# Kernel tuning notes

Measured on AMD Instinct MI355X. Metric: run time of the kernel, lower is better.

## Reference

```python
import jax, jax.numpy as jnp
import numpy as np

K = 1024
R = 4            # grid_rows * grid_cols = 2*2
D_IN = 128
D_HID = 256
D_OUT = 64
HEADS = 4
ALPHA = 0.2      # LeakyReLU slope
SEM_TH = 0.7


def _normalize(x, axis=-1):
    # torch F.normalize: x / max(||x||, eps)
    n = jnp.linalg.norm(x, axis=axis, keepdims=True)
    return x / jnp.maximum(n, 1e-12)


def _build_adjacency(page_vectors, page_numbers):
    KR = K * R
    N = K + KR + 1
    pv = _normalize(page_vectors.astype(jnp.float32))
    ps = pv @ pv.T                                    # (K,K) cosine sims
    eye_k = jnp.eye(K, dtype=bool)
    A_pp = jnp.where((ps >= SEM_TH) & (~eye_k), ps, 0.0)
    pn = page_numbers
    adj_pn = jnp.abs(pn[:, None] - pn[None, :]) == 1  # consecutive pages
    A_pp = jnp.where(adj_pn, jnp.maximum(A_pp, 0.8), A_pp)
    g_page = jnp.arange(KR) // R                      # owning page of each region
    A_pr = (g_page[None, :] == jnp.arange(K)[:, None]).astype(jnp.float32)  # (K,KR)
    same_pg = (g_page[:, None] == g_page[None, :]) & (~jnp.eye(KR, dtype=bool))
    A_rr = jnp.where(same_pg, 0.9, 0.0)
    adj = jnp.zeros((N, N), dtype=jnp.float32)
    adj = adj.at[:K, :K].set(A_pp)
    adj = adj.at[:K, K:K + KR].set(A_pr)
    adj = adj.at[K:K + KR, :K].set(A_pr.T)
    adj = adj.at[K:K + KR, K:K + KR].set(A_rr)
    adj = adj.at[N - 1, :N - 1].set(1.0)              # query node fully connected
    adj = adj.at[:N - 1, N - 1].set(1.0)
    adj = adj + jnp.eye(N, dtype=jnp.float32)         # self loops
    adj = adj / jnp.maximum(adj.sum(axis=1, keepdims=True), 1e-8)
    return adj


def _gat_layer(h, adj, W, a_src, a_dst, concat):
    # Standard multi-head GAT: e_ij = LeakyReLU(a_src.Wh_i + a_dst.Wh_j)
    N = h.shape[0]
    H, F_out = a_src.shape
    Wh = (h @ W).reshape(N, H, F_out)
    s = jnp.einsum('nhf,hf->nh', Wh, a_src)           # (N,H)
    d = jnp.einsum('nhf,hf->nh', Wh, a_dst)
    e = jax.nn.leaky_relu(s[:, None, :] + d[None, :, :], ALPHA)  # (N,N,H)
    e = jnp.where((adj > 0)[:, :, None], e, -1e9)
    att = jax.nn.softmax(e, axis=1)
    out = jnp.einsum('ijh,jhf->ihf', att, Wh)
    if concat:
        return jax.nn.elu(out.reshape(N, H * F_out))
    return out.mean(axis=1)


def setup_inputs() -> dict:
    key = jax.random.key(0)
    ks = jax.random.split(key, 20)
    sc = 0.05
    inp = {
        'page_vectors': jax.random.normal(ks[0], (K, D_IN), jnp.float32),
        'region_vectors': jax.random.normal(ks[1], (K * R, D_IN), jnp.float32),
        'query_vector': jax.random.normal(ks[2], (D_IN,), jnp.float32),
        'page_numbers': jnp.arange(K, dtype=jnp.int64) if jax.config.jax_enable_x64 else jnp.arange(K, dtype=jnp.int32),
        'stage1_scores': jax.random.normal(ks[3], (K,), jnp.float32),
        # input_proj
        'W_in': jax.random.normal(ks[4], (D_IN, D_HID), jnp.float32) * sc,
        'b_in': jnp.zeros((D_HID,), jnp.float32),
        # GAT layer 0: in=hidden, out=hidden, concat
        'W_g0': jax.random.normal(ks[5], (D_HID, HEADS * D_HID), jnp.float32) * sc,
        'a_src0': jax.random.normal(ks[6], (HEADS, D_HID), jnp.float32) * sc,
        'a_dst0': jax.random.normal(ks[7], (HEADS, D_HID), jnp.float32) * sc,
        # GAT layer 1: in=hidden*heads, out=output_dim, average
        'W_g1': jax.random.normal(ks[8], (D_HID * HEADS, HEADS * D_OUT), jnp.float32) * sc,
        'a_src1': jax.random.normal(ks[9], (HEADS, D_OUT), jnp.float32) * sc,
        'a_dst1': jax.random.normal(ks[10], (HEADS, D_OUT), jnp.float32) * sc,
        # residual proj
        'W_res': jax.random.normal(ks[11], (D_HID, D_OUT), jnp.float32) * sc,
        'b_res': jnp.zeros((D_OUT,), jnp.float32),
        # score head
        'W_s1': jax.random.normal(ks[12], (2 * D_OUT, D_OUT), jnp.float32) * sc,
        'b_s1': jnp.zeros((D_OUT,), jnp.float32),
        'W_s2': jax.random.normal(ks[13], (D_OUT, 1), jnp.float32) * sc,
        'b_s2': jnp.zeros((1,), jnp.float32),
        'lambda_mix': jnp.asarray(0.5, jnp.float32),
    }
    return inp


def reference(page_vectors, region_vectors, query_vector, page_numbers, stage1_scores,
              W_in, b_in, W_g0, a_src0, a_dst0, W_g1, a_src1, a_dst1,
              W_res, b_res, W_s1, b_s1, W_s2, b_s2, lambda_mix):
    q = _normalize(query_vector.astype(jnp.float32)[None, :])
    node_feats = _normalize(jnp.concatenate([page_vectors, region_vectors, q], axis=0))
    adj = _build_adjacency(page_vectors, page_numbers)
    h = node_feats @ W_in + b_in
    h_res = h
    h = _gat_layer(h, adj, W_g0, a_src0, a_dst0, concat=True)
    h = _gat_layer(h, adj, W_g1, a_src1, a_dst1, concat=False)
    h = h + (h_res @ W_res + b_res)
    page_repr = h[:K]                              # (K, D_OUT)
    query_repr = h[K + K * R]                      # (D_OUT,)
    pair = jnp.concatenate([page_repr, jnp.broadcast_to(query_repr, (K, D_OUT))], axis=-1)
    delta = (jax.nn.relu(pair @ W_s1 + b_s1) @ W_s2 + b_s2)[:, 0]
    s0 = stage1_scores.astype(jnp.float32)
    s0 = (s0 - s0.min()) / (s0.max() - s0.min() + 1e-8)
    lam = jax.nn.sigmoid(lambda_mix)
    return (1.0 - lam) * s0 + lam * delta
```

## Files before the change

kernel.cpp:

```cpp
#include <hip/hip_runtime.h>
#include <math.h>

#define KPG    1024
#define KRN    4096
#define NN     5121
#define MPAD   5184
#define DIN    128
#define DHID   256
#define DOUT   64
#define NHEAD  4
#define LALPHA 0.2f
#define SEMTH  0.7f
#define QNB0   128
#define QCH0   ((NN + QNB0 - 1) / QNB0)
#define QNB1   128
#define QCH1   ((NN + QNB1 - 1) / QNB1)
#define MAXD   32
#define NBLK_NORM ((NN + 1) / 2)

typedef __bf16 bf16x8 __attribute__((ext_vector_type(8)));
typedef float  f32x4  __attribute__((ext_vector_type(4)));

__device__ __forceinline__ float wave_sum(float v){
  #pragma unroll
  for (int o = 32; o > 0; o >>= 1) v += __shfl_down(v, o, 64);
  return v;
}

__device__ __forceinline__ float lrelu(float x){ return x >= 0.f ? x : LALPHA * x; }

__device__ __forceinline__ void tobf(float v, __bf16& h, __bf16& l){
  h = (__bf16)v;
  l = (__bf16)(v - (float)h);
}

__device__ __forceinline__ void xcd_bxy(int& bx, int& by){
  int nwg = gridDim.x * gridDim.y;
  int orig = blockIdx.y * gridDim.x + blockIdx.x;
  int q = nwg >> 3, r = nwg & 7, xcd = orig & 7, idx = orig >> 3;
  int wg = (xcd < r ? xcd * (q + 1) : r * (q + 1) + (xcd - r) * q) + idx;
  bx = wg % gridDim.x;
  by = wg / gridDim.x;
}

__global__ __launch_bounds__(256) void k_prep(const float* __restrict__ pv,
                                              const float* __restrict__ rv,
                                              const float* __restrict__ qv,
                                              const float* __restrict__ Win,
                                              const float* __restrict__ Wg0,
                                              const float* __restrict__ Wg1,
                                              __bf16* __restrict__ nfH,
                                              __bf16* __restrict__ nfL,
                                              __bf16* __restrict__ WinH,
                                              __bf16* __restrict__ Wg0H,
                                              __bf16* __restrict__ Wg1H){
  __shared__ float tile[64][65];
  __shared__ float w4[4];
  int b = blockIdx.x, t = threadIdx.x;
  if (b < NBLK_NORM){
    int i = b * 2 + (t >> 7);
    int tt = t & 127;
    float x = 0.f;
    if (i < NN){
      const float* src = (i < KPG) ? pv + (size_t)i * DIN
                       : (i < KPG + KRN) ? rv + (size_t)(i - KPG) * DIN : qv;
      x = src[tt];
    }
    float ss = wave_sum(x * x);
    if ((t & 63) == 0) w4[t >> 6] = ss;
    __syncthreads();
    if (i < NN){
      int rh = t >> 7;
      float norm = sqrtf(w4[2 * rh] + w4[2 * rh + 1]);
      float y = x / fmaxf(norm, 1e-12f);
      __bf16 h, l; tobf(y, h, l);
      nfH[(size_t)i * DIN + tt] = h;
      nfL[(size_t)i * DIN + tt] = l;
    }
  } else {
    int bb = b - NBLK_NORM;
    const float* W; __bf16 *TH; int K, N, tb;
    if (bb < 8){ W = Win; TH = WinH; K = DIN;  N = DHID; tb = bb; }
    else if (bb < 72){ W = Wg0; TH = Wg0H; K = DHID; N = 1024; tb = bb - 8; }
    else { W = Wg1; TH = Wg1H; K = 1024; N = DHID; tb = bb - 72; }
    int ntx = N >> 6;
    int kb = (tb / ntx) * 64, nb = (tb % ntx) * 64;
    int rr = t >> 6, cc = t & 63;
    #pragma unroll
    for (int i = 0; i < 16; ++i){
      int k = i * 4 + rr;
      tile[k][cc] = W[(size_t)(kb + k) * N + nb + cc];
    }
    __syncthreads();
    #pragma unroll
    for (int i = 0; i < 16; ++i){
      int n = i * 4 + rr;
      TH[(size_t)(nb + n) * K + kb + cc] = (__bf16)tile[cc][n];
    }
  }
}

#define MFMA(a,b,c) __builtin_amdgcn_mfma_f32_16x16x32_bf16(a, b, c, 0, 0, 0)

struct Acc { f32x4 a00, a01, a10, a11; };

template<int K, bool X3>
__device__ __forceinline__ Acc gemm_core(const __bf16* __restrict__ AH,
                                         const __bf16* __restrict__ AL,
                                         const __bf16* __restrict__ BH,
                                         const __bf16* __restrict__ BL,
                                         int rblk, int cblk,
                                         __bf16* sm){
  int t = threadIdx.x, w = t >> 6, l = t & 63;
  int lr = l & 15, lk = l >> 4;
  __bf16* sAh = sm;
  __bf16* sBh = sm + 4096;
  __bf16* sAl = sm + 8192;
  __bf16* sBl = sm + 12288;

  int srow = t >> 3, scol = t & 7;
  int e0 = srow * 64 + ((scol ^ (srow & 7)) * 8);
  int e1 = e0 + 32 * 64;
  size_t gA0 = (size_t)(rblk + srow) * K + scol * 8;
  size_t gA1 = gA0 + (size_t)32 * K;
  size_t gB0 = (size_t)(cblk + srow) * K + scol * 8;
  size_t gB1 = gB0 + (size_t)32 * K;

  int ar0 = (w >> 1) * 32 + lr, ar1 = ar0 + 16;
  int bc0 = (w & 1) * 32 + lr,  bc1 = bc0 + 16;

  Acc acc;
  #pragma unroll
  for (int r = 0; r < 4; ++r){ acc.a00[r]=0.f; acc.a01[r]=0.f; acc.a10[r]=0.f; acc.a11[r]=0.f; }

  int4 st0, st1, st4, st5, st2, st3, st6, st7;
  st0 = *(const int4*)(AH + gA0);
  st1 = *(const int4*)(AH + gA1);
  st4 = *(const int4*)(BH + gB0);
  st5 = *(const int4*)(BH + gB1);
  if (X3){
    st2 = *(const int4*)(AL + gA0);
    st3 = *(const int4*)(AL + gA1);
    st6 = *(const int4*)(BL + gB0);
    st7 = *(const int4*)(BL + gB1);
  }

  const int NSTEP = K / 64;
  #pragma unroll 1
  for (int s = 0; s < NSTEP; ++s){
    __syncthreads();
    *(int4*)(sAh + e0) = st0;  *(int4*)(sAh + e1) = st1;
    *(int4*)(sBh + e0) = st4;  *(int4*)(sBh + e1) = st5;
    if (X3){
      *(int4*)(sAl + e0) = st2;  *(int4*)(sAl + e1) = st3;
      *(int4*)(sBl + e0) = st6;  *(int4*)(sBl + e1) = st7;
    }
    if (s + 1 < NSTEP){
      size_t ka = (size_t)(s + 1) * 64;
      st0 = *(const int4*)(AH + gA0 + ka);
      st1 = *(const int4*)(AH + gA1 + ka);
      st4 = *(const int4*)(BH + gB0 + ka);
      st5 = *(const int4*)(BH + gB1 + ka);
      if (X3){
        st2 = *(const int4*)(AL + gA0 + ka);
        st3 = *(const int4*)(AL + gA1 + ka);
        st6 = *(const int4*)(BL + gB0 + ka);
        st7 = *(const int4*)(BL + gB1 + ka);
      }
    }
    __syncthreads();
    #pragma unroll
    for (int kk = 0; kk < 2; ++kk){
      int pc = ((lk + kk * 4) ^ (lr & 7)) * 8;
      bf16x8 A0h = *(const bf16x8*)(sAh + ar0 * 64 + pc);
      bf16x8 A1h = *(const bf16x8*)(sAh + ar1 * 64 + pc);
      bf16x8 B0h = *(const bf16x8*)(sBh + bc0 * 64 + pc);
      bf16x8 B1h = *(const bf16x8*)(sBh + bc1 * 64 + pc);
      acc.a00 = MFMA(A0h, B0h, acc.a00);
      acc.a01 = MFMA(A0h, B1h, acc.a01);
      acc.a10 = MFMA(A1h, B0h, acc.a10);
      acc.a11 = MFMA(A1h, B1h, acc.a11);
      if (X3){
        bf16x8 A0l = *(const bf16x8*)(sAl + ar0 * 64 + pc);
        bf16x8 A1l = *(const bf16x8*)(sAl + ar1 * 64 + pc);
        bf16x8 B0l = *(const bf16x8*)(sBl + bc0 * 64 + pc);
        bf16x8 B1l = *(const bf16x8*)(sBl + bc1 * 64 + pc);
        acc.a00 = MFMA(A0h, B0l, acc.a00); acc.a00 = MFMA(A0l, B0h, acc.a00);
        acc.a01 = MFMA(A0h, B1l, acc.a01); acc.a01 = MFMA(A0l, B1h, acc.a01);
        acc.a10 = MFMA(A1h, B0l, acc.a10); acc.a10 = MFMA(A1l, B0h, acc.a10);
        acc.a11 = MFMA(A1h, B1l, acc.a11); acc.a11 = MFMA(A1l, B1h, acc.a11);
      }
    }
  }
  return acc;
}

template<int K, bool BIAS, bool WF32, bool WBF16>
__global__ __launch_bounds__(256) void k_gemm3(const __bf16* __restrict__ AH,
                                               const __bf16* __restrict__ BH,
                                               const float* __restrict__ bias,
                                               float* __restrict__ Cf,
                                               __bf16* __restrict__ Cb,
                                               int N){
  __shared__ __bf16 smem[8192];
  int bx, by; xcd_bxy(bx, by);
  int rblk = by * 64, cblk = bx * 64;
  Acc acc = gemm_core<K, false>(AH, nullptr, BH, nullptr, rblk, cblk, smem);
  int t = threadIdx.x, w = t >> 6, l = t & 63;
  int lr = l & 15, lk = l >> 4;
  int rb = rblk + (w >> 1) * 32 + lk * 4;
  int cb = cblk + (w & 1) * 32 + lr;
  #pragma unroll
  for (int m = 0; m < 2; ++m){
    #pragma unroll
    for (int n = 0; n < 2; ++n){
      const f32x4& a = (m == 0) ? (n == 0 ? acc.a00 : acc.a01) : (n == 0 ? acc.a10 : acc.a11);
      int col = cb + n * 16;
      float bv = BIAS ? bias[col] : 0.f;
      #pragma unroll
      for (int r = 0; r < 4; ++r){
        int row = rb + m * 16 + r;
        float v = a[r] + bv;
        size_t o = (size_t)row * N + col;
        if (WF32) Cf[o] = v;
        if (WBF16) Cb[o] = (__bf16)v;
      }
    }
  }
}

template<int K, bool BIAS, bool WF32, bool WBF16>
__global__ __launch_bounds__(512) void k_gemm3s(const __bf16* __restrict__ AH,
                                                const __bf16* __restrict__ BH,
                                                const float* __restrict__ bias,
                                                float* __restrict__ Cf,
                                                __bf16* __restrict__ Cb,
                                                int N){
  __shared__ __bf16 smem[16384];
  int bx, by; xcd_bxy(bx, by);
  int rblk = by * 64, cblk = bx * 64;
  int t = threadIdx.x, kq = t >> 8, tl = t & 255;
  int w = t >> 6, quad = w & 3, l = t & 63;
  int lr = l & 15, lk = l >> 4;
  const int KH = K / 2;
  int kbase = kq * KH;

  __bf16* sAh = smem + kq * 8192;
  __bf16* sBh = sAh + 4096;

  int srow = tl >> 3, scol = tl & 7;
  int e0 = srow * 64 + ((scol ^ (srow & 7)) * 8);
  int e1 = e0 + 32 * 64;
  size_t gA0 = (size_t)(rblk + srow) * K + kbase + scol * 8;
  size_t gA1 = gA0 + (size_t)32 * K;
  size_t gB0 = (size_t)(cblk + srow) * K + kbase + scol * 8;
  size_t gB1 = gB0 + (size_t)32 * K;

  int ar0 = (quad >> 1) * 32 + lr, ar1 = ar0 + 16;
  int bc0 = (quad & 1) * 32 + lr,  bc1 = bc0 + 16;

  Acc acc;
  #pragma unroll
  for (int r = 0; r < 4; ++r){ acc.a00[r]=0.f; acc.a01[r]=0.f; acc.a10[r]=0.f; acc.a11[r]=0.f; }

  int4 st0 = *(const int4*)(AH + gA0);
  int4 st1 = *(const int4*)(AH + gA1);
  int4 st4 = *(const int4*)(BH + gB0);
  int4 st5 = *(const int4*)(BH + gB1);

  const int NSTEP = KH / 64;
  #pragma unroll 1
  for (int s = 0; s < NSTEP; ++s){
    __syncthreads();
    *(int4*)(sAh + e0) = st0;  *(int4*)(sAh + e1) = st1;
    *(int4*)(sBh + e0) = st4;  *(int4*)(sBh + e1) = st5;
    if (s + 1 < NSTEP){
      size_t ka = (size_t)(s + 1) * 64;
      st0 = *(const int4*)(AH + gA0 + ka);
      st1 = *(const int4*)(AH + gA1 + ka);
      st4 = *(const int4*)(BH + gB0 + ka);
      st5 = *(const int4*)(BH + gB1 + ka);
    }
    __syncthreads();
    #pragma unroll
    for (int kk = 0; kk < 2; ++kk){
      int pc = ((lk + kk * 4) ^ (lr & 7)) * 8;
      bf16x8 A0h = *(const bf16x8*)(sAh + ar0 * 64 + pc);
      bf16x8 A1h = *(const bf16x8*)(sAh + ar1 * 64 + pc);
      bf16x8 B0h = *(const bf16x8*)(sBh + bc0 * 64 + pc);
      bf16x8 B1h = *(const bf16x8*)(sBh + bc1 * 64 + pc);
      acc.a00 = MFMA(A0h, B0h, acc.a00);
      acc.a01 = MFMA(A0h, B1h, acc.a01);
      acc.a10 = MFMA(A1h, B0h, acc.a10);
      acc.a11 = MFMA(A1h, B1h, acc.a11);
    }
  }

  __syncthreads();
  float* part = (float*)smem;
  int rbase = (quad >> 1) * 32, cbase = (quad & 1) * 32;
  #pragma unroll
  for (int m = 0; m < 2; ++m){
    #pragma unroll
    for (int n = 0; n < 2; ++n){
      const f32x4& a = (m == 0) ? (n == 0 ? acc.a00 : acc.a01) : (n == 0 ? acc.a10 : acc.a11);
      #pragma unroll
      for (int r = 0; r < 4; ++r)
        part[kq * 4096 + (rbase + m * 16 + lk * 4 + r) * 64 + cbase + n * 16 + lr] = a[r];
    }
  }
  __syncthreads();
  #pragma unroll
  for (int e = 0; e < 8; ++e){
    int idx = e * 512 + t;
    int row = idx >> 6, col = idx & 63;
    float v = part[idx] + part[4096 + idx];
    if (BIAS) v += bias[cblk + col];
    size_t o = (size_t)(rblk + row) * N + cblk + col;
    if (WF32) Cf[o] = v;
    if (WBF16) Cb[o] = (__bf16)v;
  }
}

__global__ __launch_bounds__(256) void k_sim3(const __bf16* __restrict__ nfH,
                                              const __bf16* __restrict__ nfL,
                                              const int* __restrict__ pn,
                                              unsigned char* __restrict__ mask){
  __shared__ __bf16 smem[16384];
  int bx, by; xcd_bxy(bx, by);
  int rblk = by * 64, cblk = bx * 64;
  Acc acc = gemm_core<DIN, true>(nfH, nfL, nfH, nfL, rblk, cblk, smem);
  int t = threadIdx.x, w = t >> 6, l = t & 63;
  int lr = l & 15, lk = l >> 4;
  int rb = rblk + (w >> 1) * 32 + lk * 4;
  int cb = cblk + (w & 1) * 32 + lr;
  #pragma unroll
  for (int m = 0; m < 2; ++m){
    #pragma unroll
    for (int n = 0; n < 2; ++n){
      const f32x4& a = (m == 0) ? (n == 0 ? acc.a00 : acc.a01) : (n == 0 ? acc.a10 : acc.a11);
      int j = cb + n * 16;
      int pnj = pn[j];
      #pragma unroll
      for (int r = 0; r < 4; ++r){
        int i = rb + m * 16 + r;
        float s = a[r];
        int d = pn[i] - pnj;
        bool mb = ((s >= SEMTH) && (j != i)) || (d == 1) || (d == -1) || (j == i);
        mask[(size_t)i * KPG + j] = mb ? 1 : 0;
      }
    }
  }
}

__global__ __launch_bounds__(64) void k_nbr(const unsigned char* __restrict__ mask,
                                            int* __restrict__ nbr,
                                            int* __restrict__ deg){
  int i = blockIdx.x, l = threadIdx.x;
  const unsigned char* mrow = mask + (size_t)i * KPG;
  int off = 0;
  #pragma unroll
  for (int c = 0; c < 16; ++c){
    int j = c * 64 + l;
    bool b = mrow[j] != 0;
    unsigned long long bal = __ballot(b);
    int pos = off + __popcll(bal & ((1ull << l) - 1ull));
    if (b && pos < MAXD) nbr[i * MAXD + pos] = j;
    off += __popcll(bal);
  }
  if (l == 0) deg[i] = (off > MAXD) ? MAXD : off;
}

__global__ __launch_bounds__(256) void k_sd0(const __bf16* __restrict__ wh,
                                             const float* __restrict__ asrc,
                                             const float* __restrict__ adst,
                                             float* __restrict__ sd){
  int n = blockIdx.x, t = threadIdx.x, hh = t >> 6, l = t & 63;
  float s = 0.f, d = 0.f;
  #pragma unroll
  for (int k = 0; k < 4; ++k){
    int idx = hh * 256 + k * 64 + l;
    float v = (float)wh[(size_t)n * 1024 + idx];
    s += v * asrc[idx];
    d += v * adst[idx];
  }
  s = wave_sum(s); d = wave_sum(d);
  if (l == 0){ sd[n * 8 + hh] = s; sd[n * 8 + 4 + hh] = d; }
}

__global__ __launch_bounds__(256) void k_gat0all(const __bf16* __restrict__ wh,
                                                 const float* __restrict__ sd,
                                                 const int* __restrict__ nbr,
                                                 const int* __restrict__ deg,
                                                 __bf16* __restrict__ h1H,
                                                 float* __restrict__ qpart,
                                                 float* __restrict__ qz){
  int b = blockIdx.x, t = threadIdx.x;
  if (b < QNB0){
    int bq = b;
    float sq[NHEAD];
    #pragma unroll
    for (int h = 0; h < NHEAD; ++h) sq[h] = sd[(size_t)(NN - 1) * 8 + h];
    int j0 = bq * QCH0, j1 = (j0 + QCH0 < NN) ? j0 + QCH0 : NN;
    float acc[NHEAD] = {0.f, 0.f, 0.f, 0.f};
    float z[NHEAD] = {0.f, 0.f, 0.f, 0.f};
    #pragma unroll 4
    for (int j = j0; j < j1; ++j){
      float4 d4 = *(const float4*)&sd[j * 8 + 4];
      float e0 = expf(lrelu(sq[0] + d4.x));
      float e1 = expf(lrelu(sq[1] + d4.y));
      float e2 = expf(lrelu(sq[2] + d4.z));
      float e3 = expf(lrelu(sq[3] + d4.w));
      z[0] += e0; z[1] += e1; z[2] += e2; z[3] += e3;
      size_t base = (size_t)j * 1024 + t;
      acc[0] += e0 * (float)wh[base];
      acc[1] += e1 * (float)wh[base + 256];
      acc[2] += e2 * (float)wh[base + 512];
      acc[3] += e3 * (float)wh[base + 768];
    }
    #pragma unroll
    for (int h = 0; h < NHEAD; ++h) qpart[(size_t)bq * 1024 + h * 256 + t] = acc[h];
    if (t == 0){
      #pragma unroll
      for (int h = 0; h < NHEAD; ++h) qz[bq * 4 + h] = z[h];
    }
  } else if (b < QNB0 + KPG){
    int i = b - QNB0;
    __shared__ int jl[MAXD + 5];
    __shared__ float wgt[NHEAD][MAXD + 5];
    __shared__ float izs[NHEAD];
    int nd = deg[i], cnt = nd + 5;
    if (t < cnt)
      jl[t] = (t < nd) ? nbr[i * MAXD + t]
                       : ((t < nd + 4) ? (KPG + 4 * i + (t - nd)) : (NN - 1));
    __syncthreads();
    if (t < 4 * cnt){
      int x = t >> 2, h = t & 3;
      wgt[h][x] = expf(lrelu(sd[i * 8 + h] + sd[jl[x] * 8 + 4 + h]));
    }
    __syncthreads();
    if (t < NHEAD){
      float Z = 0.f;
      for (int x = 0; x < cnt; ++x) Z += wgt[t][x];
      izs[t] = 1.f / Z;
    }
    __syncthreads();
    float acc[NHEAD] = {0.f, 0.f, 0.f, 0.f};
    #pragma unroll 4
    for (int x = 0; x < cnt; ++x){
      size_t base = (size_t)jl[x] * 1024 + t;
      #pragma unroll
      for (int h = 0; h < NHEAD; ++h) acc[h] += wgt[h][x] * (float)wh[base + h * 256];
    }
    size_t ob = (size_t)i * 1024;
    #pragma unroll
    for (int h = 0; h < NHEAD; ++h){
      float v = acc[h] * izs[h];
      v = (v > 0.f) ? v : expm1f(v);
      h1H[ob + h * 256 + t] = (__bf16)v;
    }
  } else {
    int g = b - QNB0 - KPG;
    __shared__ float wgt2[4][NHEAD][6];
    int rb = KPG + 4 * g;
    if (t < 16){
      int r = t >> 2, h = t & 3;
      int i = rb + r;
      float si = sd[i * 8 + h];
      int jx[6] = {g, rb, rb + 1, rb + 2, rb + 3, NN - 1};
      float Z = 0.f, e[6];
      #pragma unroll
      for (int x = 0; x < 6; ++x){
        e[x] = expf(lrelu(si + sd[jx[x] * 8 + 4 + h]));
        Z += e[x];
      }
      float iz = 1.f / Z;
      #pragma unroll
      for (int x = 0; x < 6; ++x) wgt2[r][h][x] = e[x] * iz;
    }
    __syncthreads();
    float acc[4][NHEAD] = {};
    int jx[6] = {g, rb, rb + 1, rb + 2, rb + 3, NN - 1};
    #pragma unroll
    for (int x = 0; x < 6; ++x){
      size_t base = (size_t)jx[x] * 1024 + t;
      #pragma unroll
      for (int h = 0; h < NHEAD; ++h){
        float v = (float)wh[base + h * 256];
        #pragma unroll
        for (int r = 0; r < 4; ++r) acc[r][h] += wgt2[r][h][x] * v;
      }
    }
    #pragma unroll
    for (int r = 0; r < 4; ++r){
      size_t ob = (size_t)(rb + r) * 1024;
      #pragma unroll
      for (int h = 0; h < NHEAD; ++h){
        float v = acc[r][h];
        v = (v > 0.f) ? v : expm1f(v);
        h1H[ob + h * 256 + t] = (__bf16)v;
      }
    }
  }
}

__global__ __launch_bounds__(256) void k_qfin0(const float* __restrict__ qpart,
                                               const float* __restrict__ qz,
                                               __bf16* __restrict__ h1H){
  int h = blockIdx.x, t = threadIdx.x;
  float s = 0.f, Z = 0.f;
  #pragma unroll 4
  for (int b = 0; b < QNB0; ++b){
    s += qpart[(size_t)b * 1024 + h * 256 + t];
    Z += qz[b * 4 + h];
  }
  float v = s / Z;
  v = (v > 0.f) ? v : expm1f(v);
  h1H[(size_t)(NN - 1) * 1024 + h * 256 + t] = (__bf16)v;
}

__global__ __launch_bounds__(256) void k_sd1(const __bf16* __restrict__ wh,
                                             const float* __restrict__ asrc,
                                             const float* __restrict__ adst,
                                             float* __restrict__ sd){
  int n = blockIdx.x, t = threadIdx.x, hh = t >> 6, l = t & 63;
  float v = (float)wh[(size_t)n * 256 + hh * 64 + l];
  float s = wave_sum(v * asrc[hh * 64 + l]);
  float d = wave_sum(v * adst[hh * 64 + l]);
  if (l == 0){ sd[n * 8 + hh] = s; sd[n * 8 + 4 + hh] = d; }
}

__global__ __launch_bounds__(256) void k_gat1all(const __bf16* __restrict__ wh,
                                                 const float* __restrict__ sd,
                                                 const int* __restrict__ nbr,
                                                 const int* __restrict__ deg,
                                                 float* __restrict__ h2,
                                                 float* __restrict__ qpart,
                                                 float* __restrict__ qz){
  int b = blockIdx.x, t = threadIdx.x, hh = t >> 6;
  if (b < QNB1){
    int bq = b;
    float sq = sd[(size_t)(NN - 1) * 8 + hh];
    int j0 = bq * QCH1, j1 = (j0 + QCH1 < NN) ? j0 + QCH1 : NN;
    float acc = 0.f, z = 0.f;
    #pragma unroll 4
    for (int j = j0; j < j1; ++j){
      float e = expf(lrelu(sq + sd[j * 8 + 4 + hh]));
      z += e;
      acc += e * (float)wh[(size_t)j * 256 + t];
    }
    qpart[(size_t)bq * 256 + t] = acc;
    if ((t & 63) == 0) qz[bq * 4 + hh] = z;
  } else {
    int i = b - QNB1;
    __shared__ int jl[MAXD + 5];
    __shared__ float wgt[NHEAD][MAXD + 5];
    __shared__ float izs[NHEAD];
    int nd = deg[i], cnt = nd + 5;
    if (t < cnt)
      jl[t] = (t < nd) ? nbr[i * MAXD + t]
                       : ((t < nd + 4) ? (KPG + 4 * i + (t - nd)) : (NN - 1));
    __syncthreads();
    if (t < 4 * cnt){
      int x = t >> 2, h = t & 3;
      wgt[h][x] = expf(lrelu(sd[i * 8 + h] + sd[jl[x] * 8 + 4 + h]));
    }
    __syncthreads();
    if (t < NHEAD){
      float Z = 0.f;
      for (int x = 0; x < cnt; ++x) Z += wgt[t][x];
      izs[t] = 1.f / Z;
    }
    __syncthreads();
    float acc = 0.f;
    #pragma unroll 4
    for (int x = 0; x < cnt; ++x)
      acc += wgt[hh][x] * (float)wh[(size_t)jl[x] * 256 + t];
    acc *= izs[hh];
    __shared__ float col[256];
    col[t] = acc;
    __syncthreads();
    if (t < 64)
      h2[(size_t)i * 64 + t] = 0.25f * (col[t] + col[64 + t] + col[128 + t] + col[192 + t]);
  }
}

__global__ __launch_bounds__(256) void k_qfin1mm(const float* __restrict__ qpart,
                                                 const float* __restrict__ qz,
                                                 const float* __restrict__ s0,
                                                 float* __restrict__ h2,
                                                 float* __restrict__ mm){
  int t = threadIdx.x, hh = t >> 6;
  float mn = 1e30f, mx = -1e30f;
  for (int j = t; j < KPG; j += 256){
    float v = s0[j];
    mn = fminf(mn, v); mx = fmaxf(mx, v);
  }
  __shared__ float smn[256], smx[256];
  smn[t] = mn; smx[t] = mx;
  __syncthreads();
  for (int s = 128; s > 0; s >>= 1){
    if (t < s){ smn[t] = fminf(smn[t], smn[t + s]); smx[t] = fmaxf(smx[t], smx[t + s]); }
    __syncthreads();
  }
  if (t == 0){ mm[0] = smn[0]; mm[1] = smx[0]; }
  float s = 0.f, Z = 0.f;
  #pragma unroll 4
  for (int b = 0; b < QNB1; ++b){
    s += qpart[(size_t)b * 256 + t];
    Z += qz[b * 4 + hh];
  }
  __shared__ float col[256];
  col[t] = s / Z;
  __syncthreads();
  if (t < 64)
    h2[(size_t)KPG * 64 + t] = 0.25f * (col[t] + col[64 + t] + col[128 + t] + col[192 + t]);
}

__global__ __launch_bounds__(64) void k_score2(const float* __restrict__ h2,
                                               const float* __restrict__ hres,
                                               const float* __restrict__ Wres,
                                               const float* __restrict__ bres,
                                               const float* __restrict__ Ws1,
                                               const float* __restrict__ bs1,
                                               const float* __restrict__ Ws2,
                                               const float* __restrict__ bs2,
                                               const float* __restrict__ s0,
                                               const float* __restrict__ lmix,
                                               const float* __restrict__ mm,
                                               float* __restrict__ out){
  int i = blockIdx.x, t = threadIdx.x;
  __shared__ float hrow[DHID], hq[DHID], pg[64], qr[64];
  #pragma unroll
  for (int k = 0; k < 4; ++k){
    hrow[k * 64 + t] = hres[(size_t)i * DHID + k * 64 + t];
    hq[k * 64 + t]   = hres[(size_t)(NN - 1) * DHID + k * 64 + t];
  }
  __syncthreads();
  float ri = bres[t], rq = bres[t];
  #pragma unroll 8
  for (int d = 0; d < DHID; ++d){
    float w = Wres[d * 64 + t];
    ri += hrow[d] * w;
    rq += hq[d] * w;
  }
  pg[t] = h2[(size_t)i * 64 + t] + ri;
  qr[t] = h2[(size_t)KPG * 64 + t] + rq;
  __syncthreads();
  float z = bs1[t];
  #pragma unroll 8
  for (int d = 0; d < 64; ++d){
    z += pg[d] * Ws1[d * 64 + t];
    z += qr[d] * Ws1[(64 + d) * 64 + t];
  }
  z = fmaxf(z, 0.f);
  float v = wave_sum(z * Ws2[t]);
  if (t == 0){
    float delta = v + bs2[0];
    float mn = mm[0], mx = mm[1];
    float s0n = (s0[i] - mn) / (mx - mn + 1e-8f);
    float lam = 1.f / (1.f + expf(-lmix[0]));
    out[i] = (1.f - lam) * s0n + lam * delta;
  }
}

extern "C" void kernel_launch(void* const* d_in, const int* in_sizes, int n_in,
                              void* d_out, int out_size, void* d_ws, size_t ws_size,
                              hipStream_t stream){
  const float* pv  = (const float*)d_in[0];
  const float* rv  = (const float*)d_in[1];
  const float* qv  = (const float*)d_in[2];
  const int*   pn  = (const int*)d_in[3];
  const float* s0  = (const float*)d_in[4];
  const float* Win = (const float*)d_in[5];
  const float* bin = (const float*)d_in[6];
  const float* Wg0 = (const float*)d_in[7];
  const float* as0 = (const float*)d_in[8];
  const float* ad0 = (const float*)d_in[9];
  const float* Wg1 = (const float*)d_in[10];
  const float* as1 = (const float*)d_in[11];
  const float* ad1 = (const float*)d_in[12];
  const float* Wrs = (const float*)d_in[13];
  const float* brs = (const float*)d_in[14];
  const float* Ws1 = (const float*)d_in[15];
  const float* bs1 = (const float*)d_in[16];
  const float* Ws2 = (const float*)d_in[17];
  const float* bs2 = (const float*)d_in[18];
  const float* lmx = (const float*)d_in[19];
  float* out = (float*)d_out;

  float* ws = (float*)d_ws;
  size_t off = 0;
  __bf16* nfH = (__bf16*)(ws + off); off += (size_t)MPAD * DIN / 2;
  __bf16* nfL = (__bf16*)(ws + off); off += (size_t)MPAD * DIN / 2;
  __bf16* WinH = (__bf16*)(ws + off); off += (size_t)DHID * DIN / 2;
  __bf16* Wg0H = (__bf16*)(ws + off); off += (size_t)1024 * DHID / 2;
  __bf16* Wg1H = (__bf16*)(ws + off); off += (size_t)DHID * 1024 / 2;
  float* hres = ws + off; off += (size_t)MPAD * DHID;
  __bf16* hresH = (__bf16*)(ws + off); off += (size_t)MPAD * DHID / 2;
  __bf16* wh0H = (__bf16*)(ws + off); off += (size_t)MPAD * 1024 / 2;
  __bf16* h1H  = (__bf16*)(ws + off); off += (size_t)MPAD * 1024 / 2;
  __bf16* wh1H = (__bf16*)(ws + off); off += (size_t)MPAD * 256 / 2;
  float* sd0  = ws + off; off += (size_t)NN * 8;
  float* sd1  = ws + off; off += (size_t)NN * 8;
  float* h2   = ws + off; off += (size_t)(KPG + 1) * 64;
  float* qp0  = ws + off; off += (size_t)QNB0 * 1024;
  float* qp1  = ws + off; off += (size_t)QNB1 * 256;
  float* qz0  = ws + off; off += (size_t)QNB0 * 4;
  float* qz1  = ws + off; off += (size_t)QNB1 * 4;
  float* mm   = ws + off; off += 8;
  int*   nbr  = (int*)(ws + off); off += (size_t)KPG * MAXD;
  int*   deg  = (int*)(ws + off); off += KPG;
  unsigned char* mask = (unsigned char*)(ws + off);

  k_prep<<<NBLK_NORM + 136, 256, 0, stream>>>(pv, rv, qv, Win, Wg0, Wg1,
                                              nfH, nfL, WinH, Wg0H, Wg1H);
  k_sim3<<<dim3(16, 16), 256, 0, stream>>>(nfH, nfL, pn, mask);
  k_nbr<<<KPG, 64, 0, stream>>>(mask, nbr, deg);
  k_gemm3s<DIN, true, true, true><<<dim3(4, 81), 512, 0, stream>>>(
      nfH, WinH, bin, hres, hresH, DHID);
  k_gemm3<DHID, false, false, true><<<dim3(16, 81), 256, 0, stream>>>(
      hresH, Wg0H, nullptr, nullptr, wh0H, 1024);
  k_sd0<<<NN, 256, 0, stream>>>(wh0H, as0, ad0, sd0);
  k_gat0all<<<QNB0 + 2 * KPG, 256, 0, stream>>>(wh0H, sd0, nbr, deg, h1H, qp0, qz0);
  k_qfin0<<<NHEAD, 256, 0, stream>>>(qp0, qz0, h1H);
  k_gemm3s<1024, false, false, true><<<dim3(4, 81), 512, 0, stream>>>(
      h1H, Wg1H, nullptr, nullptr, wh1H, DHID);
  k_sd1<<<NN, 256, 0, stream>>>(wh1H, as1, ad1, sd1);
  k_gat1all<<<QNB1 + KPG, 256, 0, stream>>>(wh1H, sd1, nbr, deg, h2, qp1, qz1);
  k_qfin1mm<<<1, 256, 0, stream>>>(qp1, qz1, s0, h2, mm);
  k_score2<<<KPG, 64, 0, stream>>>(h2, hres, Wrs, brs, Ws1, bs1, Ws2, bs2, s0, lmx, mm, out);
}
```

Before: 114.1 us.

## Merge independent kernels and fold query finalization into last-block epilogues

Launches are fused horizontally: the similarity-mask GEMM runs alongside the input projection GEMM, and neighbor-list extraction runs alongside the Wg0 GEMM, each dispatched by block index. The separate query-finalization kernels are removed, and the last block to finish (tracked by an atomic counter zeroed in k_prep) performs that reduction instead. This cuts the launch count from 13 to 9 and the serialized gaps between launches. expf is also replaced with __expf. The risk is that the threadfence and atomic ordering must hold, and the fast exp is slightly less accurate.

```diff
diff --git a/kernel.cpp b/kernel.cpp
--- a/kernel.cpp
+++ b/kernel.cpp
@@ -34,13 +34,9 @@
   l = (__bf16)(v - (float)h);
 }
 
-__device__ __forceinline__ void xcd_bxy(int& bx, int& by){
-  int nwg = gridDim.x * gridDim.y;
-  int orig = blockIdx.y * gridDim.x + blockIdx.x;
+__device__ __forceinline__ int swz_lin(int orig, int nwg){
   int q = nwg >> 3, r = nwg & 7, xcd = orig & 7, idx = orig >> 3;
-  int wg = (xcd < r ? xcd * (q + 1) : r * (q + 1) + (xcd - r) * q) + idx;
-  bx = wg % gridDim.x;
-  by = wg / gridDim.x;
+  return (xcd < r ? xcd * (q + 1) : r * (q + 1) + (xcd - r) * q) + idx;
 }
 
 __global__ __launch_bounds__(256) void k_prep(const float* __restrict__ pv,
@@ -53,10 +49,12 @@
                                               __bf16* __restrict__ nfL,
                                               __bf16* __restrict__ WinH,
                                               __bf16* __restrict__ Wg0H,
-                                              __bf16* __restrict__ Wg1H){
+                                              __bf16* __restrict__ Wg1H,
+                                              unsigned int* __restrict__ gcnt){
   __shared__ float tile[64][65];
   __shared__ float w4[4];
   int b = blockIdx.x, t = threadIdx.x;
+  if (b == 0 && t < 8) gcnt[t] = 0;
   if (b < NBLK_NORM){
     int i = b * 2 + (t >> 7);
     int tt = t & 127;
@@ -195,49 +193,120 @@
   return acc;
 }
 
-template<int K, bool BIAS, bool WF32, bool WBF16>
-__global__ __launch_bounds__(256) void k_gemm3(const __bf16* __restrict__ AH,
-                                               const __bf16* __restrict__ BH,
-                                               const float* __restrict__ bias,
-                                               float* __restrict__ Cf,
-                                               __bf16* __restrict__ Cb,
-                                               int N){
+__global__ __launch_bounds__(256) void k_simhres(const __bf16* __restrict__ nfH,
+                                                 const __bf16* __restrict__ nfL,
+                                                 const int* __restrict__ pn,
+                                                 const __bf16* __restrict__ WinH,
+                                                 const float* __restrict__ bin,
+                                                 unsigned char* __restrict__ mask,
+                                                 float* __restrict__ hres,
+                                                 __bf16* __restrict__ hresH){
+  __shared__ __bf16 smem[16384];
+  int b = blockIdx.x, t = threadIdx.x;
+  int w = t >> 6, l = t & 63, lr = l & 15, lk = l >> 4;
+  if (b < 256){
+    int wg = swz_lin(b, 256);
+    int rblk = (wg >> 4) * 64, cblk = (wg & 15) * 64;
+    Acc acc = gemm_core<DIN, true>(nfH, nfL, nfH, nfL, rblk, cblk, smem);
+    int rb = rblk + (w >> 1) * 32 + lk * 4;
+    int cb = cblk + (w & 1) * 32 + lr;
+    #pragma unroll
+    for (int m = 0; m < 2; ++m){
+      #pragma unroll
+      for (int n = 0; n < 2; ++n){
+        const f32x4& a = (m == 0) ? (n == 0 ? acc.a00 : acc.a01) : (n == 0 ? acc.a10 : acc.a11);
+        int j = cb + n * 16;
+        int pnj = pn[j];
+        #pragma unroll
+        for (int r = 0; r < 4; ++r){
+          int i = rb + m * 16 + r;
+          float s = a[r];
+          int d = pn[i] - pnj;
+          bool mb = ((s >= SEMTH) && (j != i)) || (d == 1) || (d == -1) || (j == i);
+          mask[(size_t)i * KPG + j] = mb ? 1 : 0;
+        }
+      }
+    }
+  } else {
+    int bb = swz_lin(b - 256, 324);
+    int rblk = (bb >> 2) * 64, cblk = (bb & 3) * 64;
+    Acc acc = gemm_core<DIN, false>(nfH, nullptr, WinH, nullptr, rblk, cblk, smem);
+    int rb = rblk + (w >> 1) * 32 + lk * 4;
+    int cb = cblk + (w & 1) * 32 + lr;
+    #pragma unroll
+    for (int m = 0; m < 2; ++m){
+      #pragma unroll
+      for (int n = 0; n < 2; ++n){
+        const f32x4& a = (m == 0) ? (n == 0 ? acc.a00 : acc.a01) : (n == 0 ? acc.a10 : acc.a11);
+        int col = cb + n * 16;
+        float bv = bin[col];
+        #pragma unroll
+        for (int r = 0; r < 4; ++r){
+          int row = rb + m * 16 + r;
+          float v = a[r] + bv;
+          size_t o = (size_t)row * DHID + col;
+          hres[o] = v;
+          hresH[o] = (__bf16)v;
+        }
+      }
+    }
+  }
+}
+
+__global__ __launch_bounds__(256) void k_nbrwh0(const __bf16* __restrict__ hresH,
+                                                const __bf16* __restrict__ Wg0H,
+                                                const unsigned char* __restrict__ mask,
+                                                __bf16* __restrict__ wh0H,
+                                                int* __restrict__ nbr,
+                                                int* __restrict__ deg){
   __shared__ __bf16 smem[8192];
-  int bx, by; xcd_bxy(bx, by);
-  int rblk = by * 64, cblk = bx * 64;
-  Acc acc = gemm_core<K, false>(AH, nullptr, BH, nullptr, rblk, cblk, smem);
-  int t = threadIdx.x, w = t >> 6, l = t & 63;
-  int lr = l & 15, lk = l >> 4;
-  int rb = rblk + (w >> 1) * 32 + lk * 4;
-  int cb = cblk + (w & 1) * 32 + lr;
-  #pragma unroll
-  for (int m = 0; m < 2; ++m){
-    #pragma unroll
-    for (int n = 0; n < 2; ++n){
-      const f32x4& a = (m == 0) ? (n == 0 ? acc.a00 : acc.a01) : (n == 0 ? acc.a10 : acc.a11);
-      int col = cb + n * 16;
-      float bv = BIAS ? bias[col] : 0.f;
-      #pragma unroll
-      for (int r = 0; r < 4; ++r){
-        int row = rb + m * 16 + r;
-        float v = a[r] + bv;
-        size_t o = (size_t)row * N + col;
-        if (WF32) Cf[o] = v;
-        if (WBF16) Cb[o] = (__bf16)v;
-      }
-    }
-  }
-}
-
-template<int K, bool BIAS, bool WF32, bool WBF16>
+  int b = blockIdx.x, t = threadIdx.x;
+  if (b < 1296){
+    int wg = swz_lin(b, 1296);
+    int rblk = (wg >> 4) * 64, cblk = (wg & 15) * 64;
+    Acc acc = gemm_core<DHID, false>(hresH, nullptr, Wg0H, nullptr, rblk, cblk, smem);
+    int w = t >> 6, l = t & 63, lr = l & 15, lk = l >> 4;
+    int rb = rblk + (w >> 1) * 32 + lk * 4;
+    int cb = cblk + (w & 1) * 32 + lr;
+    #pragma unroll
+    for (int m = 0; m < 2; ++m){
+      #pragma unroll
+      for (int n = 0; n < 2; ++n){
+        const f32x4& a = (m == 0) ? (n == 0 ? acc.a00 : acc.a01) : (n == 0 ? acc.a10 : acc.a11);
+        int col = cb + n * 16;
+        #pragma unroll
+        for (int r = 0; r < 4; ++r)
+          wh0H[(size_t)(rb + m * 16 + r) * 1024 + col] = (__bf16)a[r];
+      }
+    }
+  } else {
+    int i = (b - 1296) * 4 + (t >> 6);
+    int l = t & 63;
+    const unsigned char* mrow = mask + (size_t)i * KPG;
+    int off = 0;
+    #pragma unroll
+    for (int c = 0; c < 16; ++c){
+      int j = c * 64 + l;
+      bool bb = mrow[j] != 0;
+      unsigned long long bal = __ballot(bb);
+      int pos = off + __popcll(bal & ((1ull << l) - 1ull));
+      if (bb && pos < MAXD) nbr[i * MAXD + pos] = j;
+      off += __popcll(bal);
+    }
+    if (l == 0) deg[i] = (off > MAXD) ? MAXD : off;
+  }
+}
+
+template<int K>
 __global__ __launch_bounds__(512) void k_gemm3s(const __bf16* __restrict__ AH,
                                                 const __bf16* __restrict__ BH,
-                                                const float* __restrict__ bias,
-                                                float* __restrict__ Cf,
                                                 __bf16* __restrict__ Cb,
                                                 int N){
   __shared__ __bf16 smem[16384];
-  int bx, by; xcd_bxy(bx, by);
+  int nwg = gridDim.x * gridDim.y;
+  int orig = blockIdx.y * gridDim.x + blockIdx.x;
+  int wg = swz_lin(orig, nwg);
+  int bx = wg % gridDim.x, by = wg / gridDim.x;
   int rblk = by * 64, cblk = bx * 64;
   int t = threadIdx.x, kq = t >> 8, tl = t & 255;
   int w = t >> 6, quad = w & 3, l = t & 63;
@@ -315,60 +384,8 @@
     int idx = e * 512 + t;
     int row = idx >> 6, col = idx & 63;
     float v = part[idx] + part[4096 + idx];
-    if (BIAS) v += bias[cblk + col];
-    size_t o = (size_t)(rblk + row) * N + cblk + col;
-    if (WF32) Cf[o] = v;
-    if (WBF16) Cb[o] = (__bf16)v;
-  }
-}
-
-__global__ __launch_bounds__(256) void k_sim3(const __bf16* __restrict__ nfH,
-                                              const __bf16* __restrict__ nfL,
-                                              const int* __restrict__ pn,
-                                              unsigned char* __restrict__ mask){
-  __shared__ __bf16 smem[16384];
-  int bx, by; xcd_bxy(bx, by);
-  int rblk = by * 64, cblk = bx * 64;
-  Acc acc = gemm_core<DIN, true>(nfH, nfL, nfH, nfL, rblk, cblk, smem);
-  int t = threadIdx.x, w = t >> 6, l = t & 63;
-  int lr = l & 15, lk = l >> 4;
-  int rb = rblk + (w >> 1) * 32 + lk * 4;
-  int cb = cblk + (w & 1) * 32 + lr;
-  #pragma unroll
-  for (int m = 0; m < 2; ++m){
-    #pragma unroll
-    for (int n = 0; n < 2; ++n){
-      const f32x4& a = (m == 0) ? (n == 0 ? acc.a00 : acc.a01) : (n == 0 ? acc.a10 : acc.a11);
-      int j = cb + n * 16;
-      int pnj = pn[j];
-      #pragma unroll
-      for (int r = 0; r < 4; ++r){
-        int i = rb + m * 16 + r;
-        float s = a[r];
-        int d = pn[i] - pnj;
-        bool mb = ((s >= SEMTH) && (j != i)) || (d == 1) || (d == -1) || (j == i);
-        mask[(size_t)i * KPG + j] = mb ? 1 : 0;
-      }
-    }
-  }
-}
-
-__global__ __launch_bounds__(64) void k_nbr(const unsigned char* __restrict__ mask,
-                                            int* __restrict__ nbr,
-                                            int* __restrict__ deg){
-  int i = blockIdx.x, l = threadIdx.x;
-  const unsigned char* mrow = mask + (size_t)i * KPG;
-  int off = 0;
-  #pragma unroll
-  for (int c = 0; c < 16; ++c){
-    int j = c * 64 + l;
-    bool b = mrow[j] != 0;
-    unsigned long long bal = __ballot(b);
-    int pos = off + __popcll(bal & ((1ull << l) - 1ull));
-    if (b && pos < MAXD) nbr[i * MAXD + pos] = j;
-    off += __popcll(bal);
-  }
-  if (l == 0) deg[i] = (off > MAXD) ? MAXD : off;
+    Cb[(size_t)(rblk + row) * N + cblk + col] = (__bf16)v;
+  }
 }
 
 __global__ __launch_bounds__(256) void k_sd0(const __bf16* __restrict__ wh,
@@ -394,7 +411,8 @@
                                                  const int* __restrict__ deg,
                                                  __bf16* __restrict__ h1H,
                                                  float* __restrict__ qpart,
-                                                 float* __restrict__ qz){
+                                                 float* __restrict__ qz,
+                                                 unsigned int* __restrict__ gcnt){
   int b = blockIdx.x, t = threadIdx.x;
   if (b < QNB0){
     int bq = b;
@@ -407,10 +425,10 @@
     #pragma unroll 4
     for (int j = j0; j < j1; ++j){
       float4 d4 = *(const float4*)&sd[j * 8 + 4];
-      float e0 = expf(lrelu(sq[0] + d4.x));
-      float e1 = expf(lrelu(sq[1] + d4.y));
-      float e2 = expf(lrelu(sq[2] + d4.z));
-      float e3 = expf(lrelu(sq[3] + d4.w));
+      float e0 = __expf(lrelu(sq[0] + d4.x));
+      float e1 = __expf(lrelu(sq[1] + d4.y));
+      float e2 = __expf(lrelu(sq[2] + d4.z));
+      float e3 = __expf(lrelu(sq[3] + d4.w));
       z[0] += e0; z[1] += e1; z[2] += e2; z[3] += e3;
       size_t base = (size_t)j * 1024 + t;
       acc[0] += e0 * (float)wh[base];
@@ -423,6 +441,24 @@
     if (t == 0){
       #pragma unroll
       for (int h = 0; h < NHEAD; ++h) qz[bq * 4 + h] = z[h];
+    }
+    __shared__ int isLast;
+    __threadfence();
+    if (t == 0) isLast = (atomicAdd(&gcnt[0], 1u) == QNB0 - 1);
+    __syncthreads();
+    if (isLast){
+      #pragma unroll
+      for (int h = 0; h < NHEAD; ++h){
+        float s = 0.f, Z = 0.f;
+        #pragma unroll 4
+        for (int bb = 0; bb < QNB0; ++bb){
+          s += qpart[(size_t)bb * 1024 + h * 256 + t];
+          Z += qz[bb * 4 + h];
+        }
+        float v = s / Z;
+        v = (v > 0.f) ? v : expm1f(v);
+        h1H[(size_t)(NN - 1) * 1024 + h * 256 + t] = (__bf16)v;
+      }
     }
   } else if (b < QNB0 + KPG){
     int i = b - QNB0;
@@ -436,7 +472,7 @@
     __syncthreads();
     if (t < 4 * cnt){
       int x = t >> 2, h = t & 3;
-      wgt[h][x] = expf(lrelu(sd[i * 8 + h] + sd[jl[x] * 8 + 4 + h]));
+      wgt[h][x] = __expf(lrelu(sd[i * 8 + h] + sd[jl[x] * 8 + 4 + h]));
     }
     __syncthreads();
     if (t < NHEAD){
@@ -471,7 +507,7 @@
       float Z = 0.f, e[6];
       #pragma unroll
       for (int x = 0; x < 6; ++x){
-        e[x] = expf(lrelu(si + sd[jx[x] * 8 + 4 + h]));
+        e[x] = __expf(lrelu(si + sd[jx[x] * 8 + 4 + h]));
         Z += e[x];
       }
       float iz = 1.f / Z;
@@ -502,21 +538,6 @@
       }
     }
   }
-}
-
-__global__ __launch_bounds__(256) void k_qfin0(const float* __restrict__ qpart,
-                                               const float* __restrict__ qz,
-                                               __bf16* __restrict__ h1H){
-  int h = blockIdx.x, t = threadIdx.x;
-  float s = 0.f, Z = 0.f;
-  #pragma unroll 4
-  for (int b = 0; b < QNB0; ++b){
-    s += qpart[(size_t)b * 1024 + h * 256 + t];
-    Z += qz[b * 4 + h];
-  }
-  float v = s / Z;
-  v = (v > 0.f) ? v : expm1f(v);
-  h1H[(size_t)(NN - 1) * 1024 + h * 256 + t] = (__bf16)v;
 }
 
 __global__ __launch_bounds__(256) void k_sd1(const __bf16* __restrict__ wh,
@@ -534,9 +555,12 @@
                                                  const float* __restrict__ sd,
                                                  const int* __restrict__ nbr,
                                                  const int* __restrict__ deg,
+                                                 const float* __restrict__ s0,
                                                  float* __restrict__ h2,
                                                  float* __restrict__ qpart,
-                                                 float* __restrict__ qz){
+                                                 float* __restrict__ qz,
+                                                 float* __restrict__ mm,
+                                                 unsigned int* __restrict__ gcnt){
   int b = blockIdx.x, t = threadIdx.x, hh = t >> 6;
   if (b < QNB1){
     int bq = b;
@@ -545,12 +569,42 @@
     float acc = 0.f, z = 0.f;
     #pragma unroll 4
     for (int j = j0; j < j1; ++j){
-      float e = expf(lrelu(sq + sd[j * 8 + 4 + hh]));
+      float e = __expf(lrelu(sq + sd[j * 8 + 4 + hh]));
       z += e;
       acc += e * (float)wh[(size_t)j * 256 + t];
     }
     qpart[(size_t)bq * 256 + t] = acc;
     if ((t & 63) == 0) qz[bq * 4 + hh] = z;
+    __shared__ int isLast;
+    __threadfence();
+    if (t == 0) isLast = (atomicAdd(&gcnt[1], 1u) == QNB1 - 1);
+    __syncthreads();
+    if (isLast){
+      float mn = 1e30f, mx = -1e30f;
+      for (int j = t; j < KPG; j += 256){
+        float v = s0[j];
+        mn = fminf(mn, v); mx = fmaxf(mx, v);
+      }
+      __shared__ float smn[256], smx[256];
+      smn[t] = mn; smx[t] = mx;
+      __syncthreads();
+      for (int s = 128; s > 0; s >>= 1){
+        if (t < s){ smn[t] = fminf(smn[t], smn[t + s]); smx[t] = fmaxf(smx[t], smx[t + s]); }
+        __syncthreads();
+      }
+      if (t == 0){ mm[0] = smn[0]; mm[1] = smx[0]; }
+      float s = 0.f, Z = 0.f;
+      #pragma unroll 4
+      for (int bb = 0; bb < QNB1; ++bb){
+        s += qpart[(size_t)bb * 256 + t];
+        Z += qz[bb * 4 + hh];
+      }
+      __shared__ float col[256];
+      col[t] = s / Z;
+      __syncthreads();
+      if (t < 64)
+        h2[(size_t)KPG * 64 + t] = 0.25f * (col[t] + col[64 + t] + col[128 + t] + col[192 + t]);
+    }
   } else {
     int i = b - QNB1;
     __shared__ int jl[MAXD + 5];
@@ -563,7 +617,7 @@
     __syncthreads();
     if (t < 4 * cnt){
       int x = t >> 2, h = t & 3;
-      wgt[h][x] = expf(lrelu(sd[i * 8 + h] + sd[jl[x] * 8 + 4 + h]));
+      wgt[h][x] = __expf(lrelu(sd[i * 8 + h] + sd[jl[x] * 8 + 4 + h]));
     }
     __syncthreads();
     if (t < NHEAD){
@@ -583,38 +637,6 @@
     if (t < 64)
       h2[(size_t)i * 64 + t] = 0.25f * (col[t] + col[64 + t] + col[128 + t] + col[192 + t]);
   }
-}
-
-__global__ __launch_bounds__(256) void k_qfin1mm(const float* __restrict__ qpart,
-                                                 const float* __restrict__ qz,
-                                                 const float* __restrict__ s0,
-                                                 float* __restrict__ h2,
-                                                 float* __restrict__ mm){
-  int t = threadIdx.x, hh = t >> 6;
-  float mn = 1e30f, mx = -1e30f;
-  for (int j = t; j < KPG; j += 256){
-    float v = s0[j];
-    mn = fminf(mn, v); mx = fmaxf(mx, v);
-  }
-  __shared__ float smn[256], smx[256];
-  smn[t] = mn; smx[t] = mx;
-  __syncthreads();
-  for (int s = 128; s > 0; s >>= 1){
-    if (t < s){ smn[t] = fminf(smn[t], smn[t + s]); smx[t] = fmaxf(smx[t], smx[t + s]); }
-    __syncthreads();
-  }
-  if (t == 0){ mm[0] = smn[0]; mm[1] = smx[0]; }
-  float s = 0.f, Z = 0.f;
-  #pragma unroll 4
-  for (int b = 0; b < QNB1; ++b){
-    s += qpart[(size_t)b * 256 + t];
-    Z += qz[b * 4 + hh];
-  }
-  __shared__ float col[256];
-  col[t] = s / Z;
-  __syncthreads();
-  if (t < 64)
-    h2[(size_t)KPG * 64 + t] = 0.25f * (col[t] + col[64 + t] + col[128 + t] + col[192 + t]);
 }
 
 __global__ __launch_bounds__(64) void k_score2(const float* __restrict__ h2,
@@ -659,7 +681,7 @@
     float delta = v + bs2[0];
     float mn = mm[0], mx = mm[1];
     float s0n = (s0[i] - mn) / (mx - mn + 1e-8f);
-    float lam = 1.f / (1.f + expf(-lmix[0]));
+    float lam = 1.f / (1.f + __expf(-lmix[0]));
     out[i] = (1.f - lam) * s0n + lam * delta;
   }
 }
@@ -709,25 +731,19 @@
   float* qz0  = ws + off; off += (size_t)QNB0 * 4;
   float* qz1  = ws + off; off += (size_t)QNB1 * 4;
   float* mm   = ws + off; off += 8;
+  unsigned int* gcnt = (unsigned int*)(ws + off); off += 8;
   int*   nbr  = (int*)(ws + off); off += (size_t)KPG * MAXD;
   int*   deg  = (int*)(ws + off); off += KPG;
   unsigned char* mask = (unsigned char*)(ws + off);
 
   k_prep<<<NBLK_NORM + 136, 256, 0, stream>>>(pv, rv, qv, Win, Wg0, Wg1,
-                                              nfH, nfL, WinH, Wg0H, Wg1H);
-  k_sim3<<<dim3(16, 16), 256, 0, stream>>>(nfH, nfL, pn, mask);
-  k_nbr<<<KPG, 64, 0, stream>>>(mask, nbr, deg);
-  k_gemm3s<DIN, true, true, true><<<dim3(4, 81), 512, 0, stream>>>(
-      nfH, WinH, bin, hres, hresH, DHID);
-  k_gemm3<DHID, false, false, true><<<dim3(16, 81), 256, 0, stream>>>(
-      hresH, Wg0H, nullptr, nullptr, wh0H, 1024);
+                                              nfH, nfL, WinH, Wg0H, Wg1H, gcnt);
+  k_simhres<<<256 + 324, 256, 0, stream>>>(nfH, nfL, pn, WinH, bin, mask, hres, hresH);
+  k_nbrwh0<<<1296 + 256, 256, 0, stream>>>(hresH, Wg0H, mask, wh0H, nbr, deg);
   k_sd0<<<NN, 256, 0, stream>>>(wh0H, as0, ad0, sd0);
-  k_gat0all<<<QNB0 + 2 * KPG, 256, 0, stream>>>(wh0H, sd0, nbr, deg, h1H, qp0, qz0);
-  k_qfin0<<<NHEAD, 256, 0, stream>>>(qp0, qz0, h1H);
-  k_gemm3s<1024, false, false, true><<<dim3(4, 81), 512, 0, stream>>>(
-      h1H, Wg1H, nullptr, nullptr, wh1H, DHID);
+  k_gat0all<<<QNB0 + 2 * KPG, 256, 0, stream>>>(wh0H, sd0, nbr, deg, h1H, qp0, qz0, gcnt);
+  k_gemm3s<1024><<<dim3(4, 81), 512, 0, stream>>>(h1H, Wg1H, wh1H, DHID);
   k_sd1<<<NN, 256, 0, stream>>>(wh1H, as1, ad1, sd1);
-  k_gat1all<<<QNB1 + KPG, 256, 0, stream>>>(wh1H, sd1, nbr, deg, h2, qp1, qz1);
-  k_qfin1mm<<<1, 256, 0, stream>>>(qp1, qz1, s0, h2, mm);
+  k_gat1all<<<QNB1 + KPG, 256, 0, stream>>>(wh1H, sd1, nbr, deg, s0, h2, qp1, qz1, mm, gcnt);
   k_score2<<<KPG, 64, 0, stream>>>(h2, hres, Wrs, brs, Ws1, bs1, Ws2, bs2, s0, lmx, mm, out);
 }
```

New measurement: 155.5 us. 1.36x slower.
